# Kernel tuning notes

Hardware: AMD Instinct MI355X
Metric: run time of the kernel (lower is better)

The kernel has to match this reference:

```python
import math
import jax, jax.numpy as jnp
import numpy as np

B, T, FDIM, ODIM = 16, 16, 64, 8
NQ, LAYERS, DEGREE = 10, 2, 3
NA = 4                      # ceil(log2(T))
TOT = NQ + NA               # 14 total wires
NROTS = 4 * NQ * LAYERS     # 80 params per timestep
QROTS = 4 * NQ              # 40 (qff circuit, 1 layer)
C64 = jnp.complex64


def ry_mat(t):
    c = jnp.cos(0.5 * t).astype(C64)
    s = jnp.sin(0.5 * t).astype(C64)
    return jnp.stack([jnp.stack([c, -s], -1), jnp.stack([s, c], -1)], -2)


def rz_mat(t):
    p = jnp.exp(-0.5j * t.astype(C64))
    q = jnp.exp(0.5j * t.astype(C64))
    z = jnp.zeros_like(p)
    return jnp.stack([jnp.stack([p, z], -1), jnp.stack([z, q], -1)], -2)


def crx_mat(t):
    c = jnp.cos(0.5 * t).astype(C64)
    s = (-1j) * jnp.sin(0.5 * t).astype(C64)
    z = jnp.zeros_like(c)
    o = jnp.ones_like(c)
    r0 = jnp.stack([o, z, z, z], -1)
    r1 = jnp.stack([z, o, z, z], -1)
    r2 = jnp.stack([z, z, c, s], -1)
    r3 = jnp.stack([z, z, s, c], -1)
    return jnp.stack([r0, r1, r2, r3], -2)


CNOT = jnp.array([[1, 0, 0, 0], [0, 1, 0, 0], [0, 0, 0, 1], [0, 0, 1, 0]], dtype=C64)


def apply_gate(state, U, wires):
    # state: (Be, 2,...,2) tensor; wire w lives on axis w+1. U: (2^k,2^k) or (Be,2^k,2^k)
    k = len(wires)
    axes = [w + 1 for w in wires]
    st = jnp.moveaxis(state, axes, list(range(1, k + 1)))
    shp = st.shape
    st = st.reshape(shp[0], 2 ** k, -1)
    eq = 'bij,bjr->bir' if U.ndim == 3 else 'ij,bjr->bir'
    st = jnp.einsum(eq, U, st).reshape(shp)
    return jnp.moveaxis(st, list(range(1, k + 1)), axes)


def sim14_seq(nq, layers):
    # gate sequence of Sim et al. circuit 14: RY ring, CRX ring, RY ring, CRX counter-ring
    seq, idx = [], 0
    for _ in range(layers):
        for i in range(nq):
            seq.append(('ry', (i,), idx)); idx += 1
        for i in range(nq - 1, -1, -1):
            seq.append(('crx', (i, (i + 1) % nq), idx)); idx += 1
        for i in range(nq):
            seq.append(('ry', (i,), idx)); idx += 1
        for i in [nq - 1] + list(range(nq - 1)):
            seq.append(('crx', (i, (i - 1) % nq), idx)); idx += 1
    return seq


def apply_sim14(state, params, layers, adjoint=False):
    seq = sim14_seq(NQ, layers)
    if adjoint:
        seq = seq[::-1]
    sign = -1.0 if adjoint else 1.0
    for kind, w, pidx in seq:
        th = sign * params[..., pidx]
        U = ry_mat(th) if kind == 'ry' else crx_mat(th)
        state = apply_gate(state, U, list(w))
    return state


def apply_prepare(state, prep_p, adjoint=False):
    # learnable PREPARE ansatz on ancilla wires NQ..NQ+NA-1 (n_prep_layers == NA)
    seq = []
    for ly in range(NA):
        for qi in range(NA):
            seq.append(('ry', NQ + qi, (ly, qi, 0)))
            seq.append(('rz', NQ + qi, (ly, qi, 1)))
        for i in range(NA - 1):
            seq.append(('cnot', (NQ + i, NQ + i + 1), None))
    if adjoint:
        seq = seq[::-1]
    sign = -1.0 if adjoint else 1.0
    for kind, w, pix in seq:
        if kind == 'cnot':
            state = apply_gate(state, CNOT, list(w))
        else:
            th = sign * prep_p[pix]
            U = ry_mat(th) if kind == 'ry' else rz_mat(th)
            state = apply_gate(state, U, [w])
    return state


def pcphase(state, phi):
    # PennyLane PCPhase(phi, dim=2^NQ, wires=anc+main): e^{+i phi} on ancilla==0 subspace, e^{-i phi} elsewhere
    st = state.reshape(B, 2 ** NQ, 2 ** NA)
    ph = jnp.exp(1j * phi.astype(C64))
    vec = jnp.where(jnp.arange(2 ** NA) == 0, ph, jnp.conj(ph))
    return (st * vec).reshape((B,) + (2,) * TOT)


def apply_select(state, ts_params, adjoint=False):
    # Select: apply sim14(ts_params[:, j]) on main wires when ancilla register == j
    # (T == 2^NA so there is no identity padding). Vectorized over batch x ancilla index.
    st = state.reshape(B, 2 ** NQ, 2 ** NA)
    st = jnp.moveaxis(st, 2, 1).reshape((B * T,) + (2,) * NQ)
    st = apply_sim14(st, ts_params.reshape(B * T, NROTS), LAYERS, adjoint)
    st = st.reshape(B, 2 ** NA, 2 ** NQ)
    return jnp.moveaxis(st, 1, 2).reshape((B,) + (2,) * TOT)


def expvals(state):
    # <X_i>, <Y_i>, <Z_i> on main wires, order X0..X9, Y0..Y9, Z0..Z9
    xs, ys, zs = [], [], []
    for i in range(NQ):
        s = jnp.moveaxis(state, i + 1, 1).reshape(B, 2, -1)
        s0, s1 = s[:, 0], s[:, 1]
        c = jnp.sum(jnp.conj(s0) * s1, axis=-1)
        xs.append(2.0 * jnp.real(c))
        ys.append(2.0 * jnp.imag(c))
        zs.append(jnp.sum(jnp.abs(s0) ** 2 - jnp.abs(s1) ** 2, axis=-1))
    return jnp.stack(xs + ys + zs, axis=1).astype(jnp.float32)  # (B, 3*NQ)


def make_pe():
    pos = np.arange(T, dtype=np.float32)[:, None]
    div = np.exp(np.arange(0, FDIM, 2, dtype=np.float32) * -(math.log(10000.0) / FDIM))
    pe = np.zeros((T, FDIM), np.float32)
    pe[:, 0::2] = np.sin(pos * div)
    pe[:, 1::2] = np.cos(pos * div[:FDIM // 2])
    return jnp.asarray(pe)


def setup_inputs():
    key = jax.random.key(0)
    ks = jax.random.split(key, 8)
    return {
        'x': jax.random.normal(ks[0], (B, FDIM, T), jnp.float32),
        'W_fp': jax.random.normal(ks[1], (NROTS, FDIM), jnp.float32) / math.sqrt(FDIM),
        'b_fp': jnp.zeros((NROTS,), jnp.float32),
        'prep_p': 0.1 * jax.random.normal(ks[2], (NA, NA, 2), jnp.float32),
        'sig_ang': 0.1 * jax.random.normal(ks[3], (DEGREE + 1,), jnp.float32),
        'qff_p': jax.random.uniform(ks[4], (QROTS,), jnp.float32),
        'W_out': jax.random.normal(ks[5], (ODIM, 3 * NQ), jnp.float32) / math.sqrt(3 * NQ),
        'b_out': jnp.zeros((ODIM,), jnp.float32),
    }


def reference(x, W_fp, b_fp, prep_p, sig_ang, qff_p, W_out, b_out):
    h = jnp.transpose(x, (0, 2, 1)) + make_pe()[None]          # (B, T, FDIM)
    ts = jax.nn.sigmoid(h @ W_fp.T + b_fp) * (2.0 * math.pi)    # (B, T, NROTS)
    # |0...0> on all 14 wires, batched
    psi = jnp.zeros((B, 2 ** TOT), C64).at[:, 0].set(1.0).reshape((B,) + (2,) * TOT)
    psi = pcphase(psi, sig_ang[0])
    for k in range(DEGREE):
        psi = apply_prepare(psi, prep_p, adjoint=False)
        psi = apply_select(psi, ts, adjoint=(k % 2 == 1))
        psi = apply_prepare(psi, prep_p, adjoint=True)
        psi = pcphase(psi, sig_ang[k + 1])
    psi = apply_sim14(psi, qff_p, layers=1, adjoint=False)      # QFF readout circuit
    exps = expvals(psi)                                         # (B, 30)
    return exps @ W_out.T + b_out                               # (B, ODIM)
```

## Files before the change

kernel.cpp:

```cpp
#include <hip/hip_runtime.h>
#include <math.h>
#include <utility>


struct Gate { int ry; int tbit; int cbit; int pidx; };
struct GateTab { Gate g[40]; };

constexpr GateTab make_gates1() {
  GateTab tb{};
  int pos = 0, idx = 0;
  for (int i = 0; i < 10; ++i) { tb.g[pos] = Gate{1, 9 - i, -1, idx}; ++pos; ++idx; }
  for (int i = 9; i >= 0; --i) { tb.g[pos] = Gate{0, 9 - ((i + 1) % 10), 9 - i, idx}; ++pos; ++idx; }
  for (int i = 0; i < 10; ++i) { tb.g[pos] = Gate{1, 9 - i, -1, idx}; ++pos; ++idx; }
  for (int k = 0; k < 10; ++k) {
    int i = (k == 0) ? 9 : (k - 1);
    tb.g[pos] = Gate{0, 9 - ((i + 9) % 10), 9 - i, idx}; ++pos; ++idx;
  }
  return tb;
}
constexpr GateTab GTC = make_gates1();

__device__ __forceinline__ int insert_zero(int v, int p) {
  return ((v >> p) << (p + 1)) | (v & ((1 << p) - 1));
}
__device__ __forceinline__ float2 cmul(float2 A, float2 B) {
  return make_float2(A.x * B.x - A.y * B.y, A.x * B.y + A.y * B.x);
}
__device__ __forceinline__ float2 conj2(float2 A) { return make_float2(A.x, -A.y); }

template<int XM>
__device__ __forceinline__ float lxor(float v) {
  if constexpr (XM == 1) {
    int r = __builtin_amdgcn_update_dpp(__float_as_int(v), __float_as_int(v),
                                        0xB1, 0xF, 0xF, true);
    return __int_as_float(r);
  } else if constexpr (XM == 2) {
    int r = __builtin_amdgcn_update_dpp(__float_as_int(v), __float_as_int(v),
                                        0x4E, 0xF, 0xF, true);
    return __int_as_float(r);
  } else if constexpr (XM == 8) {
    int r = __builtin_amdgcn_update_dpp(__float_as_int(v), __float_as_int(v),
                                        0x128, 0xF, 0xF, true);
    return __int_as_float(r);
  } else if constexpr (XM == 16) {
#if __has_builtin(__builtin_amdgcn_permlane16_swap)
    unsigned uv = __float_as_uint(v);
    auto r = __builtin_amdgcn_permlane16_swap(uv, uv, false, false);
    return __uint_as_float(r[0] ^ r[1] ^ uv);
#else
    return __shfl_xor(v, 16, 64);
#endif
  } else if constexpr (XM == 32) {
#if __has_builtin(__builtin_amdgcn_permlane32_swap)
    unsigned uv = __float_as_uint(v);
    auto r = __builtin_amdgcn_permlane32_swap(uv, uv, false, false);
    return __uint_as_float(r[0] ^ r[1] ^ uv);
#else
    return __shfl_xor(v, 32, 64);
#endif
  } else {
    return __shfl_xor(v, XM, 64);
  }
}

__device__ __forceinline__ float wave_sum(float v) {
  v += lxor<1>(v);
  v += lxor<2>(v);
  v += lxor<4>(v);
  v += lxor<8>(v);
  v += lxor<16>(v);
  v += lxor<32>(v);
  return v;
}

struct alignas(128) GBar {
  unsigned cnt;
  unsigned gen;
  unsigned done;
  unsigned pad[29];
};
__device__ GBar g_gb[16];

__device__ __forceinline__ void group_barrier16(int b, int lane) {
  unsigned snap = __hip_atomic_load(&g_gb[b].gen, __ATOMIC_RELAXED, __HIP_MEMORY_SCOPE_AGENT);
  if (lane == 0) {
    unsigned old = __hip_atomic_fetch_add(&g_gb[b].cnt, 1u, __ATOMIC_ACQ_REL,
                                          __HIP_MEMORY_SCOPE_AGENT);
    if ((old & 15u) == 15u)
      __hip_atomic_store(&g_gb[b].gen, snap + 1u, __ATOMIC_RELEASE,
                         __HIP_MEMORY_SCOPE_AGENT);
  }
  while (__hip_atomic_load(&g_gb[b].gen, __ATOMIC_RELAXED, __HIP_MEMORY_SCOPE_AGENT) == snap)
    __builtin_amdgcn_s_sleep(1);
  (void)__hip_atomic_load(&g_gb[b].gen, __ATOMIC_ACQUIRE, __HIP_MEMORY_SCOPE_AGENT);
}

template<int P>
__device__ __forceinline__ void ry_gate(float2 (&a)[16], float c, float s, int lane) {
  if constexpr (P < 4) {
    constexpr int m = 1 << P;
#pragma unroll
    for (int r0 = 0; r0 < 16; ++r0) {
      if (!(r0 & m)) {
        int r1 = r0 | m;
        float2 a0 = a[r0], a1 = a[r1];
        a[r0] = make_float2(c * a0.x - s * a1.x, c * a0.y - s * a1.y);
        a[r1] = make_float2(s * a0.x + c * a1.x, s * a0.y + c * a1.y);
      }
    }
  } else {
    constexpr int xm = 1 << (P - 4);
    bool up = (lane >> (P - 4)) & 1;
    float sg = up ? s : -s;
#pragma unroll
    for (int r = 0; r < 16; ++r) {
      float wx = lxor<xm>(a[r].x);
      float wy = lxor<xm>(a[r].y);
      a[r].x = c * a[r].x + sg * wx;
      a[r].y = c * a[r].y + sg * wy;
    }
  }
}

template<int P, int Q>
__device__ __forceinline__ void crx_gate(float2 (&a)[16], float c, float s, int lane) {
  if constexpr (P < 4) {
    constexpr int m = 1 << P;
#pragma unroll
    for (int r0 = 0; r0 < 16; ++r0) {
      if (!(r0 & m)) {
        int r1 = r0 | m;
        bool act;
        if constexpr (Q < 4) act = (r0 >> Q) & 1;
        else act = (lane >> (Q - 4)) & 1;
        if (act) {
          float2 a0 = a[r0], a1 = a[r1];
          a[r0] = make_float2(c * a0.x + s * a1.y, c * a0.y - s * a1.x);
          a[r1] = make_float2(c * a1.x + s * a0.y, c * a1.y - s * a0.x);
        }
      }
    }
  } else {
    constexpr int xm = 1 << (P - 4);
#pragma unroll
    for (int r = 0; r < 16; ++r) {
      float wx = lxor<xm>(a[r].x);
      float wy = lxor<xm>(a[r].y);
      bool act;
      if constexpr (Q < 4) act = (r >> Q) & 1;
      else act = (lane >> (Q - 4)) & 1;
      if (act) {
        float nx = c * a[r].x + s * wy;
        float ny = c * a[r].y - s * wx;
        a[r].x = nx; a[r].y = ny;
      }
    }
  }
}

template<bool ADJ, int G>
__device__ __forceinline__ void one_gate(float2 (&a)[16], const float2 (&sc)[40], int lane) {
  constexpr Gate g = GTC.g[ADJ ? (39 - G) : G];
  float2 scv = sc[g.pidx];
  float s = ADJ ? -scv.x : scv.x;
  float c = scv.y;
  if constexpr (g.ry != 0) ry_gate<g.tbit>(a, c, s, lane);
  else crx_gate<g.tbit, g.cbit>(a, c, s, lane);
}

template<bool ADJ, int... I>
__device__ __forceinline__ void run_layer_impl(float2 (&a)[16], const float2 (&sc)[40],
                                               int lane, std::integer_sequence<int, I...>) {
  (one_gate<ADJ, I>(a, sc, lane), ...);
}

template<bool ADJ>
__device__ __forceinline__ void run_layer(float2 (&a)[16], const float2* sc, int lane) {
  float2 rsc[40];
#pragma unroll
  for (int i = 0; i < 40; ++i) rsc[i] = sc[i];
  run_layer_impl<ADJ>(a, rsc, lane, std::make_integer_sequence<int, 40>{});
}

__global__ __launch_bounds__(256, 1) void k_fused(const float* __restrict__ x,
                                                  const float* __restrict__ W_fp,
                                                  const float* __restrict__ b_fp,
                                                  const float* __restrict__ prep,
                                                  const float* __restrict__ sig,
                                                  const float* __restrict__ qff,
                                                  const float* __restrict__ W_out,
                                                  const float* __restrict__ b_out,
                                                  float* __restrict__ out,
                                                  float4* __restrict__ part1,
                                                  float4* __restrict__ part2,
                                                  float* __restrict__ sv) {
  int blk = blockIdx.x;
  int b = blk >> 2, sub = blk & 3;
  int tid = threadIdx.x;
  int w = tid >> 6, lane = tid & 63;
  int aa = sub * 4 + w;

  __shared__ __align__(16) float h[4][64];
  __shared__ float2 scs[4][80];
  __shared__ float2 qscs[40];
  __shared__ float2 ps[32];
  __shared__ float2 es[4];
  __shared__ float2 u0s[16];
  __shared__ float4 R[2][512];

  if (sub == 0 && w == 0 && lane < 30) sv[b * 30 + lane] = 0.f;

  {
    int f = lane, k = f >> 1;
    float div = expf(-(float)(2 * k) * (logf(10000.f) / 64.f));
    float ang = (float)aa * div;
    float pe = (f & 1) ? cosf(ang) : sinf(ang);
    h[w][f] = x[(b * 64 + f) * 16 + aa] + pe;
  }
  if (w == 0) {
    if (lane < 32) {
      float s, c;
      sincosf(0.5f * prep[lane], &s, &c);
      ps[lane] = make_float2(s, c);
    } else if (lane < 36) {
      float s, c;
      sincosf(sig[lane - 32], &s, &c);
      es[lane - 32] = make_float2(c, s);
    }
  } else if (w == 1 && lane < 40) {
    float s, c;
    sincosf(0.5f * qff[lane], &s, &c);
    qscs[lane] = make_float2(s, c);
  }
  __syncthreads();

  if (w == 0) {
    float2 v[16];
#pragma unroll
    for (int i = 0; i < 16; ++i) v[i] = make_float2(i == 0 ? 1.f : 0.f, 0.f);
    for (int ly = 0; ly < 4; ++ly) {
#pragma unroll
      for (int qi = 0; qi < 4; ++qi) {
        int p = 3 - qi;
        float2 rc = ps[ly * 8 + qi * 2 + 0];
        {
          float s = rc.x, c = rc.y;
#pragma unroll
          for (int m = 0; m < 8; ++m) {
            int a0 = insert_zero(m, p), a1 = a0 | (1 << p);
            float2 t0 = v[a0], t1 = v[a1];
            v[a0] = make_float2(c * t0.x - s * t1.x, c * t0.y - s * t1.y);
            v[a1] = make_float2(s * t0.x + c * t1.x, s * t0.y + c * t1.y);
          }
        }
        rc = ps[ly * 8 + qi * 2 + 1];
        {
          float s = rc.x, c = rc.y;
#pragma unroll
          for (int m = 0; m < 8; ++m) {
            int a0 = insert_zero(m, p), a1 = a0 | (1 << p);
            float2 t0 = v[a0], t1 = v[a1];
            v[a0] = make_float2(c * t0.x + s * t0.y, c * t0.y - s * t0.x);
            v[a1] = make_float2(c * t1.x - s * t1.y, c * t1.y + s * t1.x);
          }
        }
      }
#pragma unroll
      for (int i = 0; i < 3; ++i) {
        int pc = 3 - i, pt = 2 - i;
#pragma unroll
        for (int m = 0; m < 4; ++m) {
          int mm = insert_zero(m, pt);
          mm = insert_zero(mm, pc);
          int a0 = mm | (1 << pc), a1 = a0 | (1 << pt);
          float2 t0 = v[a0], t1 = v[a1];
          v[a0] = t1; v[a1] = t0;
        }
      }
    }
    if (lane == 0) {
#pragma unroll
      for (int i = 0; i < 16; ++i) u0s[i] = v[i];
    }
  }

  {
    const float4* h4 = (const float4*)&h[w][0];
    for (int j = lane; j < 80; j += 64) {
      float acc = b_fp[j];
      const float4* w4 = (const float4*)(W_fp + j * 64);
#pragma unroll
      for (int k4 = 0; k4 < 16; ++k4) {
        float4 hh = h4[k4], ww = w4[k4];
        acc += hh.x * ww.x + hh.y * ww.y + hh.z * ww.z + hh.w * ww.w;
      }
      float sg = 1.f / (1.f + expf(-acc));
      float s, c;
      sincosf(sg * 3.14159265358979323846f, &s, &c);
      scs[w][j] = make_float2(s, c);
    }
  }
  __syncthreads();

  float2 u0aa = u0s[aa];
  float2 e0 = es[0], e1 = es[1], e2 = es[2];
  float2 m0  = cmul(u0aa, e0);
  float2 cu0 = conj2(u0aa);
  float2 ceA = conj2(e1);
  float2 wA  = make_float2(-2.f * e1.y * u0aa.y, 2.f * e1.y * u0aa.x);
  float2 ceB = conj2(e2);
  float2 wB  = make_float2(-2.f * e2.y * u0aa.y, 2.f * e2.y * u0aa.x);

  const float2* sc = &scs[w][0];
  float2 a[16];
#pragma unroll
  for (int r = 0; r < 16; ++r) a[r] = make_float2(0.f, 0.f);
  if (lane == 0) a[0] = m0;

  for (int k = 0; k < 4; ++k) {
    if (k == 1 || k == 2) {
      float2 ce = (k == 1) ? ceA : ceB;
      float2 wk = (k == 1) ? wA : wB;
      float4* part = (k == 1) ? part1 : part2;

      __syncthreads();
      if (w < 2) {
#pragma unroll
        for (int q = 0; q < 8; ++q) {
          float2 p0 = cmul(cu0, a[2 * q]);
          float2 p1 = cmul(cu0, a[2 * q + 1]);
          R[w][q * 64 + lane] = make_float4(p0.x, p0.y, p1.x, p1.y);
        }
      }
      __syncthreads();
      if (w >= 2) {
#pragma unroll
        for (int q = 0; q < 8; ++q) {
          float4 v = R[w - 2][q * 64 + lane];
          float2 p0 = cmul(cu0, a[2 * q]);
          float2 p1 = cmul(cu0, a[2 * q + 1]);
          R[w - 2][q * 64 + lane] =
              make_float4(v.x + p0.x, v.y + p0.y, v.z + p1.x, v.w + p1.y);
        }
      }
      __syncthreads();
#pragma unroll
      for (int qq = 0; qq < 2; ++qq) {
        int q = w * 2 + qq;
        float4 v0 = R[0][q * 64 + lane];
        float4 v1 = R[1][q * 64 + lane];
        part[(size_t)(b * 4 + sub) * 512 + q * 64 + lane] =
            make_float4(v0.x + v1.x, v0.y + v1.y, v0.z + v1.z, v0.w + v1.w);
      }
      group_barrier16(b, lane);

      float4 s4[8];
#pragma unroll
      for (int q = 0; q < 8; ++q) {
        float4 v0 = R[0][q * 64 + lane];
        float4 v1 = R[1][q * 64 + lane];
        s4[q] = make_float4(v0.x + v1.x, v0.y + v1.y, v0.z + v1.z, v0.w + v1.w);
      }
      for (int o = 1; o < 4; ++o) {
        int so = (sub + o) & 3;
        const float4* pp = part + (size_t)(b * 4 + so) * 512 + lane;
#pragma unroll
        for (int q = 0; q < 8; ++q) {
          float4 v = pp[q * 64];
          s4[q].x += v.x; s4[q].y += v.y; s4[q].z += v.z; s4[q].w += v.w;
        }
      }
#pragma unroll
      for (int q = 0; q < 8; ++q) {
        float2 a0 = a[2 * q], a1 = a[2 * q + 1];
        a[2 * q] = make_float2(ce.x * a0.x - ce.y * a0.y + wk.x * s4[q].x - wk.y * s4[q].y,
                               ce.x * a0.y + ce.y * a0.x + wk.x * s4[q].y + wk.y * s4[q].x);
        a[2 * q + 1] = make_float2(ce.x * a1.x - ce.y * a1.y + wk.x * s4[q].z - wk.y * s4[q].w,
                                   ce.x * a1.y + ce.y * a1.x + wk.x * s4[q].w + wk.y * s4[q].z);
      }
    }
    if (k == 1) {
#pragma unroll 1
      for (int L = 0; L < 2; ++L) run_layer<true>(a, sc + 40 * (1 - L), lane);
    } else {
      const float2* scp = (k == 3) ? &qscs[0] : sc;
      int nL = (k == 3) ? 1 : 2;
#pragma unroll 1
      for (int L = 0; L < nL; ++L) run_layer<false>(a, scp + 40 * L, lane);
    }
  }

  {
    float obs[30];
#pragma unroll
    for (int p = 0; p <= 9; ++p) {
      int i = 9 - p;
      float cr = 0.f, ci = 0.f, zz = 0.f;
      if (p < 4) {
        int m = 1 << p;
#pragma unroll
        for (int r0 = 0; r0 < 16; ++r0) {
          if (!(r0 & m)) {
            float2 A0 = a[r0], A1 = a[r0 | m];
            cr += A0.x * A1.x + A0.y * A1.y;
            ci += A0.x * A1.y - A0.y * A1.x;
            zz += (A0.x * A0.x + A0.y * A0.y) - (A1.x * A1.x + A1.y * A1.y);
          }
        }
      } else {
        int xm = 1 << (p - 4);
        bool up = (lane >> (p - 4)) & 1;
#pragma unroll
        for (int r = 0; r < 16; ++r) {
          float wx = __shfl_xor(a[r].x, xm, 64);
          float wy = __shfl_xor(a[r].y, xm, 64);
          float n2 = a[r].x * a[r].x + a[r].y * a[r].y;
          if (!up) {
            cr += a[r].x * wx + a[r].y * wy;
            ci += a[r].x * wy - a[r].y * wx;
            zz += n2;
          } else {
            zz -= n2;
          }
        }
      }
      obs[i] = 2.f * cr;
      obs[10 + i] = 2.f * ci;
      obs[20 + i] = zz;
    }
#pragma unroll
    for (int j = 0; j < 30; ++j) obs[j] = wave_sum(obs[j]);

    float* Rf = (float*)R;
    __syncthreads();
    if (lane == 0) {
#pragma unroll
      for (int j = 0; j < 30; ++j) Rf[w * 30 + j] = obs[j];
    }
    __syncthreads();
    if (w == 0) {
      if (lane < 30) {
        float v = Rf[0 * 30 + lane] + Rf[1 * 30 + lane] +
                  Rf[2 * 30 + lane] + Rf[3 * 30 + lane];
        atomicAdd(&sv[b * 30 + lane], v);
      }
      int lastflag = 0;
      if (lane == 0) {
        unsigned old = __hip_atomic_fetch_add(&g_gb[b].done, 1u, __ATOMIC_ACQ_REL,
                                              __HIP_MEMORY_SCOPE_AGENT);
        lastflag = ((old & 3u) == 3u) ? 1 : 0;
      }
      lastflag = __shfl(lastflag, 0, 64);
      if (lastflag) {
        (void)__hip_atomic_load(&g_gb[b].done, __ATOMIC_ACQUIRE, __HIP_MEMORY_SCOPE_AGENT);
        if (lane < 8) {
          float acc = b_out[lane];
#pragma unroll
          for (int j = 0; j < 30; ++j) acc += W_out[lane * 30 + j] * sv[b * 30 + j];
          out[b * 8 + lane] = acc;
        }
      }
    }
  }
}

extern "C" void kernel_launch(void* const* d_in, const int* in_sizes, int n_in,
                              void* d_out, int out_size, void* d_ws, size_t ws_size,
                              hipStream_t stream) {
  const float* x     = (const float*)d_in[0];
  const float* W_fp  = (const float*)d_in[1];
  const float* b_fp  = (const float*)d_in[2];
  const float* prep  = (const float*)d_in[3];
  const float* sig   = (const float*)d_in[4];
  const float* qff   = (const float*)d_in[5];
  const float* W_out = (const float*)d_in[6];
  const float* b_out = (const float*)d_in[7];
  float* out = (float*)d_out;
  (void)in_sizes; (void)n_in; (void)out_size;

  char* ws = (char*)d_ws;
  const size_t SZ_PART = (size_t)64 * 512 * 16;
  float4* part1 = (float4*)ws;
  float4* part2 = (float4*)(ws + SZ_PART);
  float*  sv    = (float*)(ws + 2 * SZ_PART);
  (void)ws_size;

  k_fused<<<dim3(64), dim3(256), 0, stream>>>(x, W_fp, b_fp, prep, sig, qff,
                                              W_out, b_out, out, part1, part2, sv);
}
```

Baseline: 170.3 us.

## Use packed float2 vectors for gate math and flatten layer loop into phases

Switches the per-lane amplitude registers to ext_vector_type float2 so gate updates can lower to packed FP32 instructions (v_pk_fma/v_pk_mul). The nested k/L loops are flattened into one non-unrolled 7-phase loop with a single run_layer instantiation per direction, and several small loops get unroll 1. The aim is fewer ALU instructions and less instruction-cache pressure from code duplication, at the cost of per-phase branch selection and possible packing/unpacking moves.

```diff
diff --git a/kernel.cpp b/kernel.cpp
--- a/kernel.cpp
+++ b/kernel.cpp
@@ -2,6 +2,8 @@
 #include <math.h>
 #include <utility>
 
+
+typedef float v2f __attribute__((ext_vector_type(2)));
 
 struct Gate { int ry; int tbit; int cbit; int pidx; };
 struct GateTab { Gate g[40]; };
@@ -27,6 +29,7 @@
   return make_float2(A.x * B.x - A.y * B.y, A.x * B.y + A.y * B.x);
 }
 __device__ __forceinline__ float2 conj2(float2 A) { return make_float2(A.x, -A.y); }
+__device__ __forceinline__ v2f vmk(float x, float y) { v2f r; r.x = x; r.y = y; return r; }
 
 template<int XM>
 __device__ __forceinline__ float lxor(float v) {
@@ -62,6 +65,10 @@
     return __shfl_xor(v, XM, 64);
   }
 }
+template<int XM>
+__device__ __forceinline__ v2f lxor2(v2f v) {
+  v2f r; r.x = lxor<XM>(v.x); r.y = lxor<XM>(v.y); return r;
+}
 
 __device__ __forceinline__ float wave_sum(float v) {
   v += lxor<1>(v);
@@ -96,16 +103,16 @@
 }
 
 template<int P>
-__device__ __forceinline__ void ry_gate(float2 (&a)[16], float c, float s, int lane) {
+__device__ __forceinline__ void ry_gate(v2f (&a)[16], float c, float s, int lane) {
   if constexpr (P < 4) {
     constexpr int m = 1 << P;
 #pragma unroll
     for (int r0 = 0; r0 < 16; ++r0) {
       if (!(r0 & m)) {
         int r1 = r0 | m;
-        float2 a0 = a[r0], a1 = a[r1];
-        a[r0] = make_float2(c * a0.x - s * a1.x, c * a0.y - s * a1.y);
-        a[r1] = make_float2(s * a0.x + c * a1.x, s * a0.y + c * a1.y);
+        v2f a0 = a[r0], a1 = a[r1];
+        a[r0] = c * a0 - s * a1;
+        a[r1] = s * a0 + c * a1;
       }
     }
   } else {
@@ -114,16 +121,14 @@
     float sg = up ? s : -s;
 #pragma unroll
     for (int r = 0; r < 16; ++r) {
-      float wx = lxor<xm>(a[r].x);
-      float wy = lxor<xm>(a[r].y);
-      a[r].x = c * a[r].x + sg * wx;
-      a[r].y = c * a[r].y + sg * wy;
+      v2f wv = lxor2<xm>(a[r]);
+      a[r] = c * a[r] + sg * wv;
     }
   }
 }
 
 template<int P, int Q>
-__device__ __forceinline__ void crx_gate(float2 (&a)[16], float c, float s, int lane) {
+__device__ __forceinline__ void crx_gate(v2f (&a)[16], float c, float s, int lane) {
   if constexpr (P < 4) {
     constexpr int m = 1 << P;
 #pragma unroll
@@ -134,9 +139,9 @@
         if constexpr (Q < 4) act = (r0 >> Q) & 1;
         else act = (lane >> (Q - 4)) & 1;
         if (act) {
-          float2 a0 = a[r0], a1 = a[r1];
-          a[r0] = make_float2(c * a0.x + s * a1.y, c * a0.y - s * a1.x);
-          a[r1] = make_float2(c * a1.x + s * a0.y, c * a1.y - s * a0.x);
+          v2f a0 = a[r0], a1 = a[r1];
+          a[r0] = c * a0 + s * vmk(a1.y, -a1.x);
+          a[r1] = c * a1 + s * vmk(a0.y, -a0.x);
         }
       }
     }
@@ -144,22 +149,17 @@
     constexpr int xm = 1 << (P - 4);
 #pragma unroll
     for (int r = 0; r < 16; ++r) {
-      float wx = lxor<xm>(a[r].x);
-      float wy = lxor<xm>(a[r].y);
+      v2f wv = lxor2<xm>(a[r]);
       bool act;
       if constexpr (Q < 4) act = (r >> Q) & 1;
       else act = (lane >> (Q - 4)) & 1;
-      if (act) {
-        float nx = c * a[r].x + s * wy;
-        float ny = c * a[r].y - s * wx;
-        a[r].x = nx; a[r].y = ny;
-      }
+      if (act) a[r] = c * a[r] + s * vmk(wv.y, -wv.x);
     }
   }
 }
 
 template<bool ADJ, int G>
-__device__ __forceinline__ void one_gate(float2 (&a)[16], const float2 (&sc)[40], int lane) {
+__device__ __forceinline__ void one_gate(v2f (&a)[16], const float2 (&sc)[40], int lane) {
   constexpr Gate g = GTC.g[ADJ ? (39 - G) : G];
   float2 scv = sc[g.pidx];
   float s = ADJ ? -scv.x : scv.x;
@@ -169,13 +169,13 @@
 }
 
 template<bool ADJ, int... I>
-__device__ __forceinline__ void run_layer_impl(float2 (&a)[16], const float2 (&sc)[40],
+__device__ __forceinline__ void run_layer_impl(v2f (&a)[16], const float2 (&sc)[40],
                                                int lane, std::integer_sequence<int, I...>) {
   (one_gate<ADJ, I>(a, sc, lane), ...);
 }
 
 template<bool ADJ>
-__device__ __forceinline__ void run_layer(float2 (&a)[16], const float2* sc, int lane) {
+__device__ __forceinline__ void run_layer(v2f (&a)[16], const float2* sc, int lane) {
   float2 rsc[40];
 #pragma unroll
   for (int i = 0; i < 40; ++i) rsc[i] = sc[i];
@@ -238,6 +238,7 @@
     float2 v[16];
 #pragma unroll
     for (int i = 0; i < 16; ++i) v[i] = make_float2(i == 0 ? 1.f : 0.f, 0.f);
+#pragma unroll 1
     for (int ly = 0; ly < 4; ++ly) {
 #pragma unroll
       for (int qi = 0; qi < 4; ++qi) {
@@ -312,23 +313,24 @@
   float2 wB  = make_float2(-2.f * e2.y * u0aa.y, 2.f * e2.y * u0aa.x);
 
   const float2* sc = &scs[w][0];
-  float2 a[16];
-#pragma unroll
-  for (int r = 0; r < 16; ++r) a[r] = make_float2(0.f, 0.f);
-  if (lane == 0) a[0] = m0;
-
-  for (int k = 0; k < 4; ++k) {
-    if (k == 1 || k == 2) {
-      float2 ce = (k == 1) ? ceA : ceB;
-      float2 wk = (k == 1) ? wA : wB;
-      float4* part = (k == 1) ? part1 : part2;
+  v2f a[16];
+#pragma unroll
+  for (int r = 0; r < 16; ++r) a[r] = vmk(0.f, 0.f);
+  if (lane == 0) a[0] = vmk(m0.x, m0.y);
+
+#pragma unroll 1
+  for (int ph = 0; ph < 7; ++ph) {
+    if (ph == 2 || ph == 4) {
+      float2 ce = (ph == 2) ? ceA : ceB;
+      float2 wk = (ph == 2) ? wA : wB;
+      float4* part = (ph == 2) ? part1 : part2;
 
       __syncthreads();
       if (w < 2) {
 #pragma unroll
         for (int q = 0; q < 8; ++q) {
-          float2 p0 = cmul(cu0, a[2 * q]);
-          float2 p1 = cmul(cu0, a[2 * q + 1]);
+          float2 p0 = cmul(cu0, make_float2(a[2 * q].x, a[2 * q].y));
+          float2 p1 = cmul(cu0, make_float2(a[2 * q + 1].x, a[2 * q + 1].y));
           R[w][q * 64 + lane] = make_float4(p0.x, p0.y, p1.x, p1.y);
         }
       }
@@ -337,8 +339,8 @@
 #pragma unroll
         for (int q = 0; q < 8; ++q) {
           float4 v = R[w - 2][q * 64 + lane];
-          float2 p0 = cmul(cu0, a[2 * q]);
-          float2 p1 = cmul(cu0, a[2 * q + 1]);
+          float2 p0 = cmul(cu0, make_float2(a[2 * q].x, a[2 * q].y));
+          float2 p1 = cmul(cu0, make_float2(a[2 * q + 1].x, a[2 * q + 1].y));
           R[w - 2][q * 64 + lane] =
               make_float4(v.x + p0.x, v.y + p0.y, v.z + p1.x, v.w + p1.y);
         }
@@ -361,6 +363,7 @@
         float4 v1 = R[1][q * 64 + lane];
         s4[q] = make_float4(v0.x + v1.x, v0.y + v1.y, v0.z + v1.z, v0.w + v1.w);
       }
+#pragma unroll 1
       for (int o = 1; o < 4; ++o) {
         int so = (sub + o) & 3;
         const float4* pp = part + (size_t)(b * 4 + so) * 512 + lane;
@@ -372,22 +375,18 @@
       }
 #pragma unroll
       for (int q = 0; q < 8; ++q) {
-        float2 a0 = a[2 * q], a1 = a[2 * q + 1];
-        a[2 * q] = make_float2(ce.x * a0.x - ce.y * a0.y + wk.x * s4[q].x - wk.y * s4[q].y,
-                               ce.x * a0.y + ce.y * a0.x + wk.x * s4[q].y + wk.y * s4[q].x);
-        a[2 * q + 1] = make_float2(ce.x * a1.x - ce.y * a1.y + wk.x * s4[q].z - wk.y * s4[q].w,
-                                   ce.x * a1.y + ce.y * a1.x + wk.x * s4[q].w + wk.y * s4[q].z);
-      }
-    }
-    if (k == 1) {
-#pragma unroll 1
-      for (int L = 0; L < 2; ++L) run_layer<true>(a, sc + 40 * (1 - L), lane);
-    } else {
-      const float2* scp = (k == 3) ? &qscs[0] : sc;
-      int nL = (k == 3) ? 1 : 2;
-#pragma unroll 1
-      for (int L = 0; L < nL; ++L) run_layer<false>(a, scp + 40 * L, lane);
-    }
+        v2f a0 = a[2 * q], a1 = a[2 * q + 1];
+        a[2 * q] = vmk(ce.x * a0.x - ce.y * a0.y + wk.x * s4[q].x - wk.y * s4[q].y,
+                       ce.x * a0.y + ce.y * a0.x + wk.x * s4[q].y + wk.y * s4[q].x);
+        a[2 * q + 1] = vmk(ce.x * a1.x - ce.y * a1.y + wk.x * s4[q].z - wk.y * s4[q].w,
+                           ce.x * a1.y + ce.y * a1.x + wk.x * s4[q].w + wk.y * s4[q].z);
+      }
+    }
+    const float2* scp;
+    if (ph == 6) scp = &qscs[0];
+    else scp = sc + ((ph == 1 || ph == 2 || ph == 5) ? 40 : 0);
+    if (ph == 2 || ph == 3) run_layer<true>(a, scp, lane);
+    else                    run_layer<false>(a, scp, lane);
   }
 
   {
@@ -401,7 +400,7 @@
 #pragma unroll
         for (int r0 = 0; r0 < 16; ++r0) {
           if (!(r0 & m)) {
-            float2 A0 = a[r0], A1 = a[r0 | m];
+            v2f A0 = a[r0], A1 = a[r0 | m];
             cr += A0.x * A1.x + A0.y * A1.y;
             ci += A0.x * A1.y - A0.y * A1.x;
             zz += (A0.x * A0.x + A0.y * A0.y) - (A1.x * A1.x + A1.y * A1.y);
```

Result: faster. 163.5 us (-4.0%).
